# Optimization experiments

Measured on AMD Instinct MI355X. Metric: run time of the kernel, lower is better.

Reference implementation:

```python
import jax, jax.numpy as jnp
import numpy as np

B, S, D = 2, 4096, 1024
H = 16
HD = D // H  # head_dim = 64

def setup_inputs() -> dict:
    key = jax.random.key(0)
    ks = jax.random.split(key, 9)
    sc = 1.0 / np.sqrt(D)
    return {
        "X":   jax.random.normal(ks[0], (B, S, D), dtype=jnp.float32),
        "Wq":  jax.random.normal(ks[1], (D, D), dtype=jnp.float32) * sc,
        "bq":  jax.random.normal(ks[2], (D,), dtype=jnp.float32) * 0.01,
        "Wk":  jax.random.normal(ks[3], (D, D), dtype=jnp.float32) * sc,
        "bk":  jax.random.normal(ks[4], (D,), dtype=jnp.float32) * 0.01,
        "Wv":  jax.random.normal(ks[5], (D, D), dtype=jnp.float32) * sc,
        "bv":  jax.random.normal(ks[6], (D,), dtype=jnp.float32) * 0.01,
        "Wo":  jax.random.normal(ks[7], (D, D), dtype=jnp.float32) * sc,
        "bo":  jax.random.normal(ks[8], (D,), dtype=jnp.float32) * 0.01,
    }

def reference(X, Wq, bq, Wk, bk, Wv, bv, Wo, bo):
    b, s, d = X.shape
    h, hd = H, HD
    # projections
    Q = X @ Wq + bq
    K = X @ Wk + bk
    V = X @ Wv + bv
    # [b, h, s, hd]
    Q = Q.reshape(b, s, h, hd).transpose(0, 2, 1, 3)
    K = K.reshape(b, s, h, hd).transpose(0, 2, 1, 3)
    V = V.reshape(b, s, h, hd).transpose(0, 2, 1, 3)
    scale = 1.0 / jnp.sqrt(jnp.asarray(hd, dtype=X.dtype))  # sqrt(hidden/num_heads)
    scores = jnp.einsum("bhqd,bhkd->bhqk", Q, K) * scale
    attn = jax.nn.softmax(scores, axis=-1)
    out = jnp.einsum("bhqk,bhkd->bhqd", attn, V)
    out = out.transpose(0, 2, 1, 3).reshape(b, s, d)
    return out @ Wo + bo
```

## Files before the change

### kernel.cpp

```cpp
#include <hip/hip_runtime.h>

#define Bsz 2
#define Sq  4096
#define Dm  1024
#define NH  16
#define HD  64

typedef __attribute__((ext_vector_type(8))) short short8;
typedef __attribute__((ext_vector_type(4))) float f32x4;
typedef __attribute__((ext_vector_type(2))) __fp16 fp16x2;
typedef __attribute__((ext_vector_type(4))) _Float16 half4v;
typedef __attribute__((ext_vector_type(8))) _Float16 half8v;

__device__ __forceinline__ unsigned short f2bf(float x) {
    unsigned int u = __float_as_uint(x);
    u += 0x7fffu + ((u >> 16) & 1u);
    return (unsigned short)(u >> 16);
}

__device__ __forceinline__ void gl2lds16(const unsigned short* g, unsigned short* l) {
    __builtin_amdgcn_global_load_lds(
        (const __attribute__((address_space(1))) unsigned int*)g,
        (__attribute__((address_space(3))) unsigned int*)l, 16, 0, 0);
}

__global__ __launch_bounds__(256) void cvt_bf16(const float4* __restrict__ in,
                                                ushort4* __restrict__ out) {
    const int i = blockIdx.x * 256 + threadIdx.x;
    const float4 v = in[i];
    ushort4 r;
    r.x = f2bf(v.x); r.y = f2bf(v.y); r.z = f2bf(v.z); r.w = f2bf(v.w);
    out[i] = r;
}

__global__ __launch_bounds__(256) void wtrans4(const float* __restrict__ Wq,
                                               const float* __restrict__ Wk,
                                               const float* __restrict__ Wv,
                                               const float* __restrict__ Wo,
                                               unsigned short* __restrict__ WtAll) {
    __shared__ float tile[64][65];
    const int z = blockIdx.z;
    const float* W = (z == 0) ? Wq : (z == 1) ? Wk : (z == 2) ? Wv : Wo;
    unsigned short* Wt = WtAll + (size_t)z * Dm * Dm;
    const int k0 = blockIdx.y * 64, n0 = blockIdx.x * 64;
    const int t = threadIdx.x;
    #pragma unroll
    for (int i = 0; i < 16; ++i) {
        const int idx = t + i * 256, r = idx >> 6, c = idx & 63;
        tile[r][c] = W[(size_t)(k0 + r) * Dm + n0 + c];
    }
    __syncthreads();
    #pragma unroll
    for (int i = 0; i < 16; ++i) {
        const int idx = t + i * 256, rr = idx >> 6, cc = idx & 63;
        Wt[(size_t)(n0 + rr) * Dm + k0 + cc] = f2bf(tile[cc][rr]);
    }
}

struct GemmCtx {
    int wm, wn, quad, c16;
    f32x4 acc[4][4];
};

__device__ __forceinline__ void gemm_core(
    const unsigned short* __restrict__ A,
    const unsigned short* __restrict__ Bt,
    int bm, int bn, unsigned short* As, unsigned short* Bs, GemmCtx& cx)
{
    const int t    = threadIdx.x;
    const int w    = t >> 6;
    const int lane = t & 63;
    cx.quad = lane >> 4;
    cx.c16  = lane & 15;
    cx.wm = (w >> 1) * 64;
    cx.wn = (w & 1) * 64;

    #pragma unroll
    for (int i = 0; i < 4; ++i)
        #pragma unroll
        for (int j = 0; j < 4; ++j)
            cx.acc[i][j] = (f32x4){0.f, 0.f, 0.f, 0.f};

    const int srow = lane >> 2, soff = (lane & 3) * 8;
    const unsigned short* Ag0 = A  + (size_t)(bm + w * 16 + srow) * Dm + soff;
    const unsigned short* Ag1 = Ag0 + (size_t)64 * Dm;
    const unsigned short* Bg0 = Bt + (size_t)(bn + w * 16 + srow) * Dm + soff;
    const unsigned short* Bg1 = Bg0 + (size_t)64 * Dm;
    unsigned short* Al0 = As + (w * 16) * 32;
    unsigned short* Al1 = As + (64 + w * 16) * 32;
    unsigned short* Bl0 = Bs + (w * 16) * 32;
    unsigned short* Bl1 = Bs + (64 + w * 16) * 32;

    for (int k0 = 0; k0 < Dm; k0 += 32) {
        __syncthreads();
        gl2lds16(Ag0 + k0, Al0);
        gl2lds16(Ag1 + k0, Al1);
        gl2lds16(Bg0 + k0, Bl0);
        gl2lds16(Bg1 + k0, Bl1);
        __syncthreads();

        short8 af[4], bf[4];
        #pragma unroll
        for (int mt = 0; mt < 4; ++mt)
            af[mt] = *(const short8*)(As + (cx.wm + mt * 16 + cx.c16) * 32 + cx.quad * 8);
        #pragma unroll
        for (int nt = 0; nt < 4; ++nt)
            bf[nt] = *(const short8*)(Bs + (cx.wn + nt * 16 + cx.c16) * 32 + cx.quad * 8);
        #pragma unroll
        for (int mt = 0; mt < 4; ++mt)
            #pragma unroll
            for (int nt = 0; nt < 4; ++nt)
                cx.acc[mt][nt] = __builtin_amdgcn_mfma_f32_16x16x32_bf16(
                    af[mt], bf[nt], cx.acc[mt][nt], 0, 0, 0);
    }
}

__global__ __launch_bounds__(256) void gemm_qkv(
    const unsigned short* __restrict__ A,
    const unsigned short* __restrict__ WtAll,
    const float* __restrict__ bq, const float* __restrict__ bk,
    const float* __restrict__ bv,
    unsigned short* __restrict__ Qh, unsigned short* __restrict__ Kh,
    unsigned short* __restrict__ Vt, float qscale)
{
    __shared__ unsigned short As[128 * 32];
    __shared__ unsigned short Bs[128 * 32];
    const int bm = blockIdx.y * 128;
    const int bn = blockIdx.x * 128;
    GemmCtx cx;
    gemm_core(A, WtAll, bm, bn, As, Bs, cx);

    const int which = bn >> 10;
    const float* bias = (which == 0) ? bq : (which == 1) ? bk : bv;
    const float osc = (which == 0) ? qscale : 1.0f;

    #pragma unroll
    for (int mt = 0; mt < 4; ++mt) {
        const int m0 = bm + cx.wm + mt * 16 + cx.quad * 4;
        #pragma unroll
        for (int nt = 0; nt < 4; ++nt) {
            const int n  = bn + cx.wn + nt * 16 + cx.c16;
            const int nl = n & 1023;
            const float bvv = bias[nl];
            const int h = (nl >> 6), d = nl & 63;
            if (which < 2) {
                unsigned short* C = (which == 0) ? Qh : Kh;
                #pragma unroll
                for (int r = 0; r < 4; ++r) {
                    const int m = m0 + r;
                    const int b = m >> 12, s = m & (Sq - 1);
                    C[((size_t)(b * NH + h) * Sq + s) * HD + d] =
                        f2bf((cx.acc[mt][nt][r] + bvv) * osc);
                }
            } else {
                const int b = m0 >> 12, s0 = m0 & (Sq - 1);
                union { fp16x2 h2[2]; unsigned int u[2]; } pk;
                pk.h2[0] = __builtin_amdgcn_cvt_pkrtz(cx.acc[mt][nt][0] + bvv,
                                                      cx.acc[mt][nt][1] + bvv);
                pk.h2[1] = __builtin_amdgcn_cvt_pkrtz(cx.acc[mt][nt][2] + bvv,
                                                      cx.acc[mt][nt][3] + bvv);
                *(uint2*)(Vt + ((size_t)(b * NH + h) * HD + d) * Sq + s0) =
                    make_uint2(pk.u[0], pk.u[1]);
            }
        }
    }
}

__global__ __launch_bounds__(256) void gemm_o(
    const unsigned short* __restrict__ A,
    const unsigned short* __restrict__ Bt,
    const float* __restrict__ bias, float* __restrict__ C)
{
    __shared__ unsigned short As[128 * 32];
    __shared__ unsigned short Bs[128 * 32];
    const int bm = blockIdx.y * 128;
    const int bn = blockIdx.x * 128;
    GemmCtx cx;
    gemm_core(A, Bt, bm, bn, As, Bs, cx);

    #pragma unroll
    for (int mt = 0; mt < 4; ++mt) {
        const int m0 = bm + cx.wm + mt * 16 + cx.quad * 4;
        #pragma unroll
        for (int nt = 0; nt < 4; ++nt) {
            const int n = bn + cx.wn + nt * 16 + cx.c16;
            const float bvv = bias[n];
            #pragma unroll
            for (int r = 0; r < 4; ++r)
                C[(size_t)(m0 + r) * Dm + n] = cx.acc[mt][nt][r] + bvv;
        }
    }
}

__global__ __launch_bounds__(256, 2) void attn_mfma6(
    const unsigned short* __restrict__ Q,
    const unsigned short* __restrict__ K,
    const unsigned short* __restrict__ Vt,
    unsigned short* __restrict__ AO)
{
    __shared__ unsigned short Ks[2][64 * 64];
    __shared__ unsigned short Vs[2][64 * 64];

    const int qt = blockIdx.x;
    const int bh = blockIdx.y;
    const int b = bh >> 4, h = bh & 15;
    const int t    = threadIdx.x;
    const int w    = t >> 6;
    const int lane = t & 63;
    const int quad = lane >> 4;
    const int c16  = lane & 15;
    const size_t base = (size_t)bh * Sq * HD;

    short8 qf[4][2];
    #pragma unroll
    for (int qg = 0; qg < 4; ++qg) {
        const unsigned short* qp =
            Q + base + (size_t)(qt * 256 + w * 64 + qg * 16 + c16) * HD;
        qf[qg][0] = *(const short8*)(qp + quad * 8);
        qf[qg][1] = *(const short8*)(qp + 32 + quad * 8);
    }

    f32x4 O[4][4];
    f32x4 Lsum[4];
    #pragma unroll
    for (int qg = 0; qg < 4; ++qg) {
        Lsum[qg] = (f32x4){0.f, 0.f, 0.f, 0.f};
        #pragma unroll
        for (int g = 0; g < 4; ++g)
            O[qg][g] = (f32x4){0.f, 0.f, 0.f, 0.f};
    }
    half8v ones8;
    #pragma unroll
    for (int i = 0; i < 8; ++i) ones8[i] = (_Float16)1.f;

    const int srow = t >> 2, sc4 = (t & 3) * 8;
    const int swr = (srow & 7) << 3;
    const int f0 = (sc4 < 16) ? sc4 * 2 : (sc4 - 16) * 2 + 4;
    const int f1 = (sc4 + 4 < 16) ? (sc4 + 4) * 2 : (sc4 - 12) * 2 + 4;
    const int kc0 = sc4 ^ swr, kc1 = (sc4 + 32) ^ swr;
    const int vc0 = f0 ^ swr, vc1 = f1 ^ swr;
    const int vc2 = (32 + f0) ^ swr, vc3 = (32 + f1) ^ swr;

    const unsigned short* kg = K  + base + (size_t)srow * HD + sc4;
    const unsigned short* vg = Vt + base + (size_t)srow * Sq + sc4;
    unsigned short* ksl = &Ks[0][0] + srow * 64;
    unsigned short* vsl = &Vs[0][0] + srow * 64;
    const int LBUF = 64 * 64;

    int4 kr0, kr1, vr0, vr1;
    kr0 = *(const int4*)(kg);
    kr1 = *(const int4*)(kg + 32);
    vr0 = *(const int4*)(vg);
    vr1 = *(const int4*)(vg + 32);
    *(int4*)(ksl + kc0) = kr0;
    *(int4*)(ksl + kc1) = kr1;
    *(uint2*)(vsl + vc0) = make_uint2(vr0.x, vr0.y);
    *(uint2*)(vsl + vc1) = make_uint2(vr0.z, vr0.w);
    *(uint2*)(vsl + vc2) = make_uint2(vr1.x, vr1.y);
    *(uint2*)(vsl + vc3) = make_uint2(vr1.z, vr1.w);

    for (int kt = 0; kt < Sq / 64; ++kt) {
        const int cur = kt & 1;
        if (kt + 1 < Sq / 64) {
            const unsigned short* kp = kg + (size_t)(kt + 1) * 64 * HD;
            const unsigned short* vp = vg + (kt + 1) * 64;
            kr0 = *(const int4*)(kp);
            kr1 = *(const int4*)(kp + 32);
            vr0 = *(const int4*)(vp);
            vr1 = *(const int4*)(vp + 32);
        }
        __syncthreads();

        const unsigned short* ksb = &Ks[cur][0];
        const unsigned short* vsb = &Vs[cur][0];

        half4v P4[4][4];
        #pragma unroll
        for (int nt = 0; nt < 4; ++nt) {
            const int krow = nt * 16 + c16;
            const int ksw = (krow & 7) << 3;
            const short8 kf0 = *(const short8*)(ksb + krow * 64 + ((quad * 8) ^ ksw));
            const short8 kf1 = *(const short8*)(ksb + krow * 64 + ((32 + quad * 8) ^ ksw));
            #pragma unroll
            for (int qg = 0; qg < 4; ++qg) {
                f32x4 z = (f32x4){0.f, 0.f, 0.f, 0.f};
                z = __builtin_amdgcn_mfma_f32_16x16x32_bf16(kf0, qf[qg][0], z, 0, 0, 0);
                z = __builtin_amdgcn_mfma_f32_16x16x32_bf16(kf1, qf[qg][1], z, 0, 0, 0);
                const float p0 = __builtin_amdgcn_exp2f(z[0]);
                const float p1 = __builtin_amdgcn_exp2f(z[1]);
                const float p2 = __builtin_amdgcn_exp2f(z[2]);
                const float p3 = __builtin_amdgcn_exp2f(z[3]);
                union { fp16x2 h2[2]; half4v h4; } pk;
                pk.h2[0] = __builtin_amdgcn_cvt_pkrtz(p0, p1);
                pk.h2[1] = __builtin_amdgcn_cvt_pkrtz(p2, p3);
                P4[qg][nt] = pk.h4;
            }
        }

        half8v P32[4][2];
        #pragma unroll
        for (int qg = 0; qg < 4; ++qg) {
            #pragma unroll
            for (int cc = 0; cc < 2; ++cc) {
                union { half4v h4[2]; half8v h8; } u;
                u.h4[0] = P4[qg][2 * cc];
                u.h4[1] = P4[qg][2 * cc + 1];
                P32[qg][cc] = u.h8;
            }
        }

        #pragma unroll
        for (int cc = 0; cc < 2; ++cc) {
            #pragma unroll
            for (int g = 0; g < 4; ++g) {
                const int vrow = g * 16 + c16;
                const half8v vf = *(const half8v*)
                    (vsb + vrow * 64 + ((cc * 32 + quad * 8) ^ ((vrow & 7) << 3)));
                #pragma unroll
                for (int qg = 0; qg < 4; ++qg)
                    O[qg][g] = __builtin_amdgcn_mfma_f32_16x16x32_f16(
                        P32[qg][cc], vf, O[qg][g], 0, 0, 0);
            }
            #pragma unroll
            for (int qg = 0; qg < 4; ++qg)
                Lsum[qg] = __builtin_amdgcn_mfma_f32_16x16x32_f16(
                    P32[qg][cc], ones8, Lsum[qg], 0, 0, 0);
        }

        if (kt + 1 < Sq / 64) {
            const int nb = cur ^ 1;
            *(int4*)(ksl + nb * LBUF + kc0) = kr0;
            *(int4*)(ksl + nb * LBUF + kc1) = kr1;
            unsigned short* vdst = vsl + nb * LBUF;
            *(uint2*)(vdst + vc0) = make_uint2(vr0.x, vr0.y);
            *(uint2*)(vdst + vc1) = make_uint2(vr0.z, vr0.w);
            *(uint2*)(vdst + vc2) = make_uint2(vr1.x, vr1.y);
            *(uint2*)(vdst + vc3) = make_uint2(vr1.z, vr1.w);
        }
    }

    #pragma unroll
    for (int qg = 0; qg < 4; ++qg) {
        float linv[4];
        #pragma unroll
        for (int r = 0; r < 4; ++r) linv[r] = 1.f / Lsum[qg][r];
        #pragma unroll
        for (int g = 0; g < 4; ++g) {
            const int col = h * HD + g * 16 + c16;
            #pragma unroll
            for (int r = 0; r < 4; ++r) {
                const int s = qt * 256 + w * 64 + qg * 16 + quad * 4 + r;
                AO[((size_t)(b * Sq + s)) * Dm + col] = f2bf(O[qg][g][r] * linv[r]);
            }
        }
    }
}

extern "C" void kernel_launch(void* const* d_in, const int* in_sizes, int n_in,
                              void* d_out, int out_size, void* d_ws, size_t ws_size,
                              hipStream_t stream)
{
    const float* X  = (const float*)d_in[0];
    const float* Wq = (const float*)d_in[1];
    const float* bq = (const float*)d_in[2];
    const float* Wk = (const float*)d_in[3];
    const float* bk = (const float*)d_in[4];
    const float* Wv = (const float*)d_in[5];
    const float* bv = (const float*)d_in[6];
    const float* Wo = (const float*)d_in[7];
    const float* bo = (const float*)d_in[8];
    float* out = (float*)d_out;

    unsigned short* ws = (unsigned short*)d_ws;
    const size_t NX = (size_t)Bsz * Sq * Dm;
    const size_t NW = (size_t)Dm * Dm;
    unsigned short* Xb    = ws; ws += NX;
    unsigned short* WtAll = ws; ws += 4 * NW;
    unsigned short* Qh    = ws; ws += NX;
    unsigned short* Kh    = ws; ws += NX;
    unsigned short* Vt    = ws; ws += NX;
    unsigned short* AO    = ws; ws += NX;

    cvt_bf16<<<(int)(NX / 1024), 256, 0, stream>>>((const float4*)X, (ushort4*)Xb);
    wtrans4<<<dim3(16, 16, 4), 256, 0, stream>>>(Wq, Wk, Wv, Wo, WtAll);

    const float SCL = 0.18033688011112042f;
    gemm_qkv<<<dim3(3 * Dm / 128, (Bsz * Sq) / 128), 256, 0, stream>>>(
        Xb, WtAll, bq, bk, bv, Qh, Kh, Vt, SCL);

    attn_mfma6<<<dim3(Sq / 256, Bsz * NH), 256, 0, stream>>>(Qh, Kh, Vt, AO);

    gemm_o<<<dim3(Dm / 128, (Bsz * Sq) / 128), 256, 0, stream>>>(
        AO, WtAll + 3 * NW, bo, out);
}
```

Measured before the change: 319.0 us.

## Software-pipeline attention QK/exp/PV, async K loads, LDS-staged V store, remap grid

The attention kernel is restructured so QK^T MFMAs for the next key sub-tile overlap with exp2/pack of the previous one and with the PV MFMAs, using sched_barriers to pin the order. K tiles now load directly into LDS via global_load_lds, and V stores to LDS are interleaved with the Lsum MFMAs. The grid becomes 1D with a remapping of (batch-head, q-tile) so blocks sharing the same K/V are placed differently across CUs. The QKV GEMM epilogue for V now transposes through a larger padded LDS buffer and writes Vt with coalesced 16-byte stores, at the cost of extra LDS and two barriers.

```diff
diff --git a/kernel.cpp b/kernel.cpp
--- a/kernel.cpp
+++ b/kernel.cpp
@@ -123,8 +123,9 @@
     unsigned short* __restrict__ Qh, unsigned short* __restrict__ Kh,
     unsigned short* __restrict__ Vt, float qscale)
 {
-    __shared__ unsigned short As[128 * 32];
-    __shared__ unsigned short Bs[128 * 32];
+    __shared__ unsigned short Smem[128 * 144];
+    unsigned short* As = Smem;
+    unsigned short* Bs = Smem + 128 * 32;
     const int bm = blockIdx.y * 128;
     const int bn = blockIdx.x * 128;
     GemmCtx cx;
@@ -134,16 +135,16 @@
     const float* bias = (which == 0) ? bq : (which == 1) ? bk : bv;
     const float osc = (which == 0) ? qscale : 1.0f;
 
-    #pragma unroll
-    for (int mt = 0; mt < 4; ++mt) {
-        const int m0 = bm + cx.wm + mt * 16 + cx.quad * 4;
-        #pragma unroll
-        for (int nt = 0; nt < 4; ++nt) {
-            const int n  = bn + cx.wn + nt * 16 + cx.c16;
-            const int nl = n & 1023;
-            const float bvv = bias[nl];
-            const int h = (nl >> 6), d = nl & 63;
-            if (which < 2) {
+    if (which < 2) {
+        #pragma unroll
+        for (int mt = 0; mt < 4; ++mt) {
+            const int m0 = bm + cx.wm + mt * 16 + cx.quad * 4;
+            #pragma unroll
+            for (int nt = 0; nt < 4; ++nt) {
+                const int n  = bn + cx.wn + nt * 16 + cx.c16;
+                const int nl = n & 1023;
+                const float bvv = bias[nl];
+                const int h = (nl >> 6), d = nl & 63;
                 unsigned short* C = (which == 0) ? Qh : Kh;
                 #pragma unroll
                 for (int r = 0; r < 4; ++r) {
@@ -152,17 +153,37 @@
                     C[((size_t)(b * NH + h) * Sq + s) * HD + d] =
                         f2bf((cx.acc[mt][nt][r] + bvv) * osc);
                 }
-            } else {
-                const int b = m0 >> 12, s0 = m0 & (Sq - 1);
+            }
+        }
+    } else {
+        __syncthreads();
+        #pragma unroll
+        for (int mt = 0; mt < 4; ++mt) {
+            const int mloc = cx.wm + mt * 16 + cx.quad * 4;
+            #pragma unroll
+            for (int nt = 0; nt < 4; ++nt) {
+                const int nloc = cx.wn + nt * 16 + cx.c16;
+                const float bvv = bias[(bn & 1023) + nloc];
                 union { fp16x2 h2[2]; unsigned int u[2]; } pk;
                 pk.h2[0] = __builtin_amdgcn_cvt_pkrtz(cx.acc[mt][nt][0] + bvv,
                                                       cx.acc[mt][nt][1] + bvv);
                 pk.h2[1] = __builtin_amdgcn_cvt_pkrtz(cx.acc[mt][nt][2] + bvv,
                                                       cx.acc[mt][nt][3] + bvv);
-                *(uint2*)(Vt + ((size_t)(b * NH + h) * HD + d) * Sq + s0) =
-                    make_uint2(pk.u[0], pk.u[1]);
-            }
-        }
+                *(uint2*)(Smem + nloc * 144 + mloc) = make_uint2(pk.u[0], pk.u[1]);
+            }
+        }
+        __syncthreads();
+        const int t = threadIdx.x;
+        const int r2 = t >> 1, seg = t & 1;
+        const int h = ((bn - 2048) >> 6) + (r2 >> 6);
+        const int d = r2 & 63;
+        const int bb = bm >> 12;
+        unsigned short* dst = Vt + ((size_t)(bb * NH + h) * HD + d) * Sq
+                                 + (bm & (Sq - 1)) + seg * 64;
+        const unsigned short* src = Smem + r2 * 144 + seg * 64;
+        #pragma unroll
+        for (int j2 = 0; j2 < 8; ++j2)
+            *(int4*)(dst + j2 * 8) = *(const int4*)(src + j2 * 8);
     }
 }
 
@@ -192,7 +213,7 @@
     }
 }
 
-__global__ __launch_bounds__(256, 2) void attn_mfma6(
+__global__ __launch_bounds__(256, 2) void attn_mfma9(
     const unsigned short* __restrict__ Q,
     const unsigned short* __restrict__ K,
     const unsigned short* __restrict__ Vt,
@@ -201,8 +222,10 @@
     __shared__ unsigned short Ks[2][64 * 64];
     __shared__ unsigned short Vs[2][64 * 64];
 
-    const int qt = blockIdx.x;
-    const int bh = blockIdx.y;
+    const int wg  = blockIdx.x;
+    const int j   = wg >> 3;
+    const int bh  = (wg & 7) * 4 + (j >> 4);
+    const int qt  = j & 15;
     const int b = bh >> 4, h = bh & 15;
     const int t    = threadIdx.x;
     const int w    = t >> 6;
@@ -232,28 +255,30 @@
     half8v ones8;
     #pragma unroll
     for (int i = 0; i < 8; ++i) ones8[i] = (_Float16)1.f;
+    const f32x4 zero4 = (f32x4){0.f, 0.f, 0.f, 0.f};
+
+    const int lrow = lane >> 3, lchunk = lane & 7;
+    const unsigned short* kgA = K + base + (size_t)(16 * w + lrow) * HD
+                                  + (lchunk ^ lrow) * 8;
+    const unsigned short* kgB = kgA + (size_t)8 * HD;
+    unsigned short* klA = &Ks[0][0] + (16 * w) * 64;
+    unsigned short* klB = klA + 8 * 64;
 
     const int srow = t >> 2, sc4 = (t & 3) * 8;
     const int swr = (srow & 7) << 3;
     const int f0 = (sc4 < 16) ? sc4 * 2 : (sc4 - 16) * 2 + 4;
     const int f1 = (sc4 + 4 < 16) ? (sc4 + 4) * 2 : (sc4 - 12) * 2 + 4;
-    const int kc0 = sc4 ^ swr, kc1 = (sc4 + 32) ^ swr;
     const int vc0 = f0 ^ swr, vc1 = f1 ^ swr;
     const int vc2 = (32 + f0) ^ swr, vc3 = (32 + f1) ^ swr;
 
-    const unsigned short* kg = K  + base + (size_t)srow * HD + sc4;
     const unsigned short* vg = Vt + base + (size_t)srow * Sq + sc4;
-    unsigned short* ksl = &Ks[0][0] + srow * 64;
     unsigned short* vsl = &Vs[0][0] + srow * 64;
     const int LBUF = 64 * 64;
 
-    int4 kr0, kr1, vr0, vr1;
-    kr0 = *(const int4*)(kg);
-    kr1 = *(const int4*)(kg + 32);
-    vr0 = *(const int4*)(vg);
-    vr1 = *(const int4*)(vg + 32);
-    *(int4*)(ksl + kc0) = kr0;
-    *(int4*)(ksl + kc1) = kr1;
+    gl2lds16(kgA, klA);
+    gl2lds16(kgB, klB);
+    int4 vr0 = *(const int4*)(vg);
+    int4 vr1 = *(const int4*)(vg + 32);
     *(uint2*)(vsl + vc0) = make_uint2(vr0.x, vr0.y);
     *(uint2*)(vsl + vc1) = make_uint2(vr0.z, vr0.w);
     *(uint2*)(vsl + vc2) = make_uint2(vr1.x, vr1.y);
@@ -261,82 +286,126 @@
 
     for (int kt = 0; kt < Sq / 64; ++kt) {
         const int cur = kt & 1;
-        if (kt + 1 < Sq / 64) {
-            const unsigned short* kp = kg + (size_t)(kt + 1) * 64 * HD;
+        __syncthreads();
+        const int nb = cur ^ 1;
+        const bool pre = (kt + 1 < Sq / 64);
+        if (pre) {
+            const unsigned short* kp = kgA + (size_t)(kt + 1) * 64 * HD;
+            gl2lds16(kp, klA + nb * LBUF);
+            gl2lds16(kp + (size_t)8 * HD, klB + nb * LBUF);
             const unsigned short* vp = vg + (kt + 1) * 64;
-            kr0 = *(const int4*)(kp);
-            kr1 = *(const int4*)(kp + 32);
             vr0 = *(const int4*)(vp);
             vr1 = *(const int4*)(vp + 32);
         }
-        __syncthreads();
+        unsigned short* vdst = vsl + nb * LBUF;
 
         const unsigned short* ksb = &Ks[cur][0];
         const unsigned short* vsb = &Vs[cur][0];
 
-        half4v P4[4][4];
-        #pragma unroll
-        for (int nt = 0; nt < 4; ++nt) {
-            const int krow = nt * 16 + c16;
+        auto krd = [&](int nt5, short8& r0, short8& r1) {
+            const int krow = nt5 * 16 + c16;
             const int ksw = (krow & 7) << 3;
-            const short8 kf0 = *(const short8*)(ksb + krow * 64 + ((quad * 8) ^ ksw));
-            const short8 kf1 = *(const short8*)(ksb + krow * 64 + ((32 + quad * 8) ^ ksw));
-            #pragma unroll
-            for (int qg = 0; qg < 4; ++qg) {
-                f32x4 z = (f32x4){0.f, 0.f, 0.f, 0.f};
-                z = __builtin_amdgcn_mfma_f32_16x16x32_bf16(kf0, qf[qg][0], z, 0, 0, 0);
-                z = __builtin_amdgcn_mfma_f32_16x16x32_bf16(kf1, qf[qg][1], z, 0, 0, 0);
-                const float p0 = __builtin_amdgcn_exp2f(z[0]);
-                const float p1 = __builtin_amdgcn_exp2f(z[1]);
-                const float p2 = __builtin_amdgcn_exp2f(z[2]);
-                const float p3 = __builtin_amdgcn_exp2f(z[3]);
-                union { fp16x2 h2[2]; half4v h4; } pk;
-                pk.h2[0] = __builtin_amdgcn_cvt_pkrtz(p0, p1);
-                pk.h2[1] = __builtin_amdgcn_cvt_pkrtz(p2, p3);
-                P4[qg][nt] = pk.h4;
-            }
-        }
-
-        half8v P32[4][2];
-        #pragma unroll
-        for (int qg = 0; qg < 4; ++qg) {
-            #pragma unroll
-            for (int cc = 0; cc < 2; ++cc) {
-                union { half4v h4[2]; half8v h8; } u;
-                u.h4[0] = P4[qg][2 * cc];
-                u.h4[1] = P4[qg][2 * cc + 1];
-                P32[qg][cc] = u.h8;
-            }
-        }
-
-        #pragma unroll
-        for (int cc = 0; cc < 2; ++cc) {
-            #pragma unroll
-            for (int g = 0; g < 4; ++g) {
-                const int vrow = g * 16 + c16;
-                const half8v vf = *(const half8v*)
-                    (vsb + vrow * 64 + ((cc * 32 + quad * 8) ^ ((vrow & 7) << 3)));
-                #pragma unroll
-                for (int qg = 0; qg < 4; ++qg)
-                    O[qg][g] = __builtin_amdgcn_mfma_f32_16x16x32_f16(
-                        P32[qg][cc], vf, O[qg][g], 0, 0, 0);
-            }
-            #pragma unroll
-            for (int qg = 0; qg < 4; ++qg)
-                Lsum[qg] = __builtin_amdgcn_mfma_f32_16x16x32_f16(
-                    P32[qg][cc], ones8, Lsum[qg], 0, 0, 0);
-        }
-
-        if (kt + 1 < Sq / 64) {
-            const int nb = cur ^ 1;
-            *(int4*)(ksl + nb * LBUF + kc0) = kr0;
-            *(int4*)(ksl + nb * LBUF + kc1) = kr1;
-            unsigned short* vdst = vsl + nb * LBUF;
-            *(uint2*)(vdst + vc0) = make_uint2(vr0.x, vr0.y);
-            *(uint2*)(vdst + vc1) = make_uint2(vr0.z, vr0.w);
-            *(uint2*)(vdst + vc2) = make_uint2(vr1.x, vr1.y);
-            *(uint2*)(vdst + vc3) = make_uint2(vr1.z, vr1.w);
-        }
+            r0 = *(const short8*)(ksb + krow * 64 + ((quad * 8) ^ ksw));
+            r1 = *(const short8*)(ksb + krow * 64 + ((32 + quad * 8) ^ ksw));
+        };
+        auto exppack = [&](const f32x4 zv) -> half4v {
+            const float p0 = __builtin_amdgcn_exp2f(zv[0]);
+            const float p1 = __builtin_amdgcn_exp2f(zv[1]);
+            const float p2 = __builtin_amdgcn_exp2f(zv[2]);
+            const float p3 = __builtin_amdgcn_exp2f(zv[3]);
+            union { fp16x2 h2[2]; half4v h4; } pk;
+            pk.h2[0] = __builtin_amdgcn_cvt_pkrtz(p0, p1);
+            pk.h2[1] = __builtin_amdgcn_cvt_pkrtz(p2, p3);
+            return pk.h4;
+        };
+
+        short8 kA0, kA1, kB0, kB1;
+        f32x4 zA[4], zB[4];
+        half8v P32a[4], P32b[4];
+        half8v vfr[4];
+
+        auto ntstep = [&](const short8 kc0, const short8 kc1, f32x4* zw,
+                          const f32x4* zr, half8v* Pdst, const int hi) {
+            #pragma unroll
+            for (int q = 0; q < 4; ++q) {
+                zw[q] = __builtin_amdgcn_mfma_f32_16x16x32_bf16(
+                    kc0, qf[q][0], zero4, 0, 0, 0);
+                __builtin_amdgcn_sched_barrier(0);
+                ((half4v*)&Pdst[q])[hi] = exppack(zr[q]);
+                __builtin_amdgcn_sched_barrier(0);
+            }
+            #pragma unroll
+            for (int q = 0; q < 4; ++q) {
+                zw[q] = __builtin_amdgcn_mfma_f32_16x16x32_bf16(
+                    kc1, qf[q][1], zw[q], 0, 0, 0);
+                __builtin_amdgcn_sched_barrier(0);
+            }
+        };
+
+        krd(0, kA0, kA1);
+        krd(1, kB0, kB1);
+
+        #pragma unroll
+        for (int q = 0; q < 4; ++q)
+            zA[q] = __builtin_amdgcn_mfma_f32_16x16x32_bf16(
+                kA0, qf[q][0], zero4, 0, 0, 0);
+        #pragma unroll
+        for (int q = 0; q < 4; ++q)
+            zA[q] = __builtin_amdgcn_mfma_f32_16x16x32_bf16(
+                kA1, qf[q][1], zA[q], 0, 0, 0);
+        __builtin_amdgcn_sched_barrier(0);
+
+        krd(2, kA0, kA1);
+        ntstep(kB0, kB1, zB, zA, P32a, 0);
+        krd(3, kB0, kB1);
+        ntstep(kA0, kA1, zA, zB, P32a, 1);
+        #pragma unroll
+        for (int g = 0; g < 4; ++g) {
+            const int vrow = g * 16 + c16;
+            vfr[g] = *(const half8v*)
+                (vsb + vrow * 64 + ((quad * 8) ^ ((vrow & 7) << 3)));
+        }
+        ntstep(kB0, kB1, zB, zA, P32b, 0);
+
+        #pragma unroll
+        for (int g = 0; g < 4; ++g) {
+            #pragma unroll
+            for (int q = 0; q < 4; ++q)
+                O[q][g] = __builtin_amdgcn_mfma_f32_16x16x32_f16(
+                    P32a[q], vfr[g], O[q][g], 0, 0, 0);
+            __builtin_amdgcn_sched_barrier(0);
+            ((half4v*)&P32b[g])[1] = exppack(zB[g]);
+            __builtin_amdgcn_sched_barrier(0);
+            const int vrow = g * 16 + c16;
+            vfr[g] = *(const half8v*)
+                (vsb + vrow * 64 + ((32 + quad * 8) ^ ((vrow & 7) << 3)));
+            __builtin_amdgcn_sched_barrier(0);
+        }
+        #pragma unroll
+        for (int q = 0; q < 4; ++q) {
+            Lsum[q] = __builtin_amdgcn_mfma_f32_16x16x32_f16(
+                P32a[q], ones8, Lsum[q], 0, 0, 0);
+            __builtin_amdgcn_sched_barrier(0);
+            if (pre) {
+                if (q == 0) *(uint2*)(vdst + vc0) = make_uint2(vr0.x, vr0.y);
+                if (q == 1) *(uint2*)(vdst + vc1) = make_uint2(vr0.z, vr0.w);
+                if (q == 2) *(uint2*)(vdst + vc2) = make_uint2(vr1.x, vr1.y);
+                if (q == 3) *(uint2*)(vdst + vc3) = make_uint2(vr1.z, vr1.w);
+            }
+            __builtin_amdgcn_sched_barrier(0);
+        }
+        #pragma unroll
+        for (int g = 0; g < 4; ++g) {
+            #pragma unroll
+            for (int q = 0; q < 4; ++q)
+                O[q][g] = __builtin_amdgcn_mfma_f32_16x16x32_f16(
+                    P32b[q], vfr[g], O[q][g], 0, 0, 0);
+            __builtin_amdgcn_sched_barrier(0);
+        }
+        #pragma unroll
+        for (int q = 0; q < 4; ++q)
+            Lsum[q] = __builtin_amdgcn_mfma_f32_16x16x32_f16(
+                P32b[q], ones8, Lsum[q], 0, 0, 0);
     }
 
     #pragma unroll
@@ -388,7 +457,7 @@
     gemm_qkv<<<dim3(3 * Dm / 128, (Bsz * Sq) / 128), 256, 0, stream>>>(
         Xb, WtAll, bq, bk, bv, Qh, Kh, Vt, SCL);
 
-    attn_mfma6<<<dim3(Sq / 256, Bsz * NH), 256, 0, stream>>>(Qh, Kh, Vt, AO);
+    attn_mfma9<<<dim3(512), 256, 0, stream>>>(Qh, Kh, Vt, AO);
 
     gemm_o<<<dim3(Dm / 128, (Bsz * Sq) / 128), 256, 0, stream>>>(
         AO, WtAll + 3 * NW, bo, out);
```

New measurement: 337.4 us. 1.06x slower.
